# Kernel tuning notes

Measured on AMD Instinct MI355X. Metric: run time of the kernel, lower is better.

## Reference

```python
import jax, jax.numpy as jnp
import numpy as np

N_NODES = 50000
N_EDGES = 600000
N_FEAT = 64
D = 128
N_GRAPHS = 1024
N_LAYERS = 4


def setup_inputs() -> dict:
    key = jax.random.key(0)
    ks = jax.random.split(key, 16)
    x = jax.random.normal(ks[0], (N_NODES, N_FEAT), dtype=jnp.float32)
    edge_index = jax.random.randint(ks[1], (2, N_EDGES), 0, N_NODES, dtype=jnp.int64)
    batch_index = jnp.sort(jax.random.randint(ks[2], (N_NODES,), 0, N_GRAPHS, dtype=jnp.int64))
    def lin(k, fan_in, fan_out):
        s = 1.0 / np.sqrt(fan_in)
        kw, kb = jax.random.split(k)
        w = jax.random.uniform(kw, (fan_in, fan_out), minval=-s, maxval=s, dtype=jnp.float32)
        b = jax.random.uniform(kb, (fan_out,), minval=-s, maxval=s, dtype=jnp.float32)
        return w, b
    w0, b0 = lin(ks[3], N_FEAT, D)
    w1, b1 = lin(ks[4], D, D)
    w2, b2 = lin(ks[5], D, D)
    w3, b3 = lin(ks[6], D, D)
    wp, bp = lin(ks[7], D, D)
    return {"x": x, "edge_index": edge_index, "batch_index": batch_index,
            "w0": w0, "b0": b0, "w1": w1, "b1": b1, "w2": w2, "b2": b2,
            "w3": w3, "b3": b3, "wp": wp, "bp": bp}


def _gin_layer(x, src, dst, w, b):
    # GINConv with eps=0: MLP(x_i + sum_{j in N(i)} x_j); MLP = Linear -> ReLU
    agg = jax.ops.segment_sum(x[src], dst, num_segments=N_NODES)
    return jax.nn.relu((x + agg) @ w + b)


def reference(x, edge_index, batch_index, w0, b0, w1, b1, w2, b2, w3, b3, wp, bp):
    src, dst = edge_index[0], edge_index[1]
    # first layer changes width 64 -> 128; agg happens in input width
    agg0 = jax.ops.segment_sum(x[src], dst, num_segments=N_NODES)
    h = jax.nn.relu((x + agg0) @ w0 + b0)
    for w, b in ((w1, b1), (w2, b2), (w3, b3)):
        h = _gin_layer(h, src, dst, w, b)
    # global mean pool per graph
    sums = jax.ops.segment_sum(h, batch_index, num_segments=N_GRAPHS)
    counts = jax.ops.segment_sum(jnp.ones((N_NODES,), dtype=h.dtype), batch_index, num_segments=N_GRAPHS)
    pooled = sums / jnp.maximum(counts, 1.0)[:, None]
    # post_mp: Linear -> ReLU (dropout identity at inference)
    return jax.nn.relu(pooled @ wp + bp)
```

## Files before the change

kernel.cpp:

```cpp
#include <hip/hip_runtime.h>
#include <hip/hip_fp16.h>


#define N_NODES  50000
#define N_EDGES  600000
#define N_FEAT   64
#define DIM      128
#define N_GRAPHS 1024
#define NB_SCAN  49
#define NBINS    36
#define TPB      256
#define GT128    ((N_NODES + 127) / 128)

typedef _Float16 f16x8 __attribute__((ext_vector_type(8)));
typedef float    f32x4 __attribute__((ext_vector_type(4)));

#define CNTZ  (N_NODES / 4)
#define XWORK (N_NODES * N_FEAT / 4)
#define PREP_TOTAL (CNTZ + XWORK + N_FEAT * DIM + 3 * DIM * DIM)

__global__ __launch_bounds__(TPB) void prep_k(
    const float* __restrict__ x, __half* __restrict__ xh,
    const float* __restrict__ w0, const float* __restrict__ w1,
    const float* __restrict__ w2, const float* __restrict__ w3,
    __half* __restrict__ Wt0, __half* __restrict__ Wt1,
    __half* __restrict__ Wt2, __half* __restrict__ Wt3,
    int* __restrict__ cnt) {
  int i = blockIdx.x * TPB + threadIdx.x;
  if (i < CNTZ) {
    *reinterpret_cast<int4*>(cnt + i * 4) = make_int4(0, 0, 0, 0);
    return;
  }
  i -= CNTZ;
  if (i < XWORK) {
    float4 v = *reinterpret_cast<const float4*>(x + (size_t)i * 4);
    union { __half2 h2[2]; uint2 u; } pk;
    pk.h2[0] = __floats2half2_rn(v.x, v.y);
    pk.h2[1] = __floats2half2_rn(v.z, v.w);
    *reinterpret_cast<uint2*>(xh + (size_t)i * 4) = pk.u;
    return;
  }
  int j = i - XWORK;
  if (j < N_FEAT * DIM) {
    int k = j >> 7, n = j & 127;
    Wt0[n * N_FEAT + k] = __float2half(w0[j]);
    return;
  }
  j -= N_FEAT * DIM;
  if (j >= 3 * DIM * DIM) return;
  int wsel = j / (DIM * DIM);
  int jj = j - wsel * (DIM * DIM);
  int k = jj >> 7, n = jj & 127;
  const float* W = (wsel == 0) ? w1 : (wsel == 1) ? w2 : w3;
  __half* Wt     = (wsel == 0) ? Wt1 : (wsel == 1) ? Wt2 : Wt3;
  Wt[n * DIM + k] = __float2half(W[jj]);
}

__global__ __launch_bounds__(TPB) void hist_k(
    const int* __restrict__ dst, int* __restrict__ cnt) {
  int e = blockIdx.x * TPB + threadIdx.x;
  if (e < N_EDGES) atomicAdd(&cnt[dst[e]], 1);
}

__global__ __launch_bounds__(TPB) void scan_part_k(
    const int* __restrict__ cnt, int* __restrict__ part,
    int* __restrict__ bins) {
  __shared__ int ws[4];
  __shared__ int lbin[NBINS];
  int t = threadIdx.x, b = blockIdx.x;
  if (t < NBINS) lbin[t] = 0;
  __syncthreads();
  int base = b * 1024 + t * 4;
  int s = 0;
  int v[4] = {0, 0, 0, 0};
  if (base + 3 < N_NODES) {
    int4 q = *reinterpret_cast<const int4*>(cnt + base);
    v[0] = q.x; v[1] = q.y; v[2] = q.z; v[3] = q.w;
  } else {
    for (int i = 0; i < 4; ++i) if (base + i < N_NODES) v[i] = cnt[base + i];
  }
#pragma unroll
  for (int i = 0; i < 4; ++i) {
    s += v[i];
    if (base + i < N_NODES) atomicAdd(&lbin[min(v[i], NBINS - 1)], 1);
  }
  for (int off = 32; off; off >>= 1) s += __shfl_down(s, off, 64);
  int lane = t & 63, wv = t >> 6;
  if (lane == 0) ws[wv] = s;
  __syncthreads();
  if (t == 0) part[b] = ws[0] + ws[1] + ws[2] + ws[3];
  if (t < NBINS) bins[b * NBINS + t] = lbin[t];
}

__global__ __launch_bounds__(TPB) void scan_write_k(
    const int* __restrict__ cnt, const int* __restrict__ part,
    const int* __restrict__ bins, int* __restrict__ row_ptr,
    int* __restrict__ fill, int* __restrict__ node_order) {
  __shared__ int wsum[4];
  __shared__ int blk_off_s;
  __shared__ int offj[NBINS];
  __shared__ int lrank[NBINS];
  int t = threadIdx.x, b = blockIdx.x;
  int lane = t & 63, wv = t >> 6;
  int base = b * 1024 + t * 4;

  if (base + 3 < N_NODES)
    *reinterpret_cast<int4*>(fill + base) = make_int4(0, 0, 0, 0);
  else
    for (int i = 0; i < 4; ++i) if (base + i < N_NODES) fill[base + i] = 0;

  if (t < 64) {
    int v = (t < NB_SCAN) ? part[t] : 0;
    int incl = v;
    for (int off = 1; off < 64; off <<= 1) {
      int u = __shfl_up(incl, off, 64);
      if (t >= off) incl += u;
    }
    if (t == b) blk_off_s = incl - v;
  }

  int colbelow = 0, coltot = 0;
  if (t < NBINS) {
    for (int b2 = 0; b2 < NB_SCAN; ++b2) {
      int u = bins[b2 * NBINS + t];
      if (b2 < b) colbelow += u;
      coltot += u;
    }
  }
  if (t < 64) {
    int v = (t < NBINS) ? coltot : 0;
    int incl = v;
    for (int off = 1; off < 64; off <<= 1) {
      int u = __shfl_up(incl, off, 64);
      if (t >= off) incl += u;
    }
    if (t < NBINS) offj[t] = (incl - v) + colbelow;
  }
  if (t < NBINS) lrank[t] = 0;

  int v[4];
#pragma unroll
  for (int i = 0; i < 4; ++i) v[i] = (base + i < N_NODES) ? cnt[base + i] : 0;
  int ls = v[0] + v[1] + v[2] + v[3];
  int incl = ls;
  for (int off = 1; off < 64; off <<= 1) {
    int u = __shfl_up(incl, off, 64);
    if (lane >= off) incl += u;
  }
  if (lane == 63) wsum[wv] = incl;
  __syncthreads();
  int woff = 0;
  for (int w = 0; w < wv; ++w) woff += wsum[w];
  int off0 = blk_off_s + woff + (incl - ls);
  int rp0 = off0, rp1 = off0 + v[0], rp2 = rp1 + v[1], rp3 = rp2 + v[2];
  if (base + 3 < N_NODES)
    *reinterpret_cast<int4*>(row_ptr + base) = make_int4(rp0, rp1, rp2, rp3);
  else {
    int rp[4] = {rp0, rp1, rp2, rp3};
    for (int i = 0; i < 4; ++i) if (base + i < N_NODES) row_ptr[base + i] = rp[i];
  }
  if (b == 0 && t == 0) row_ptr[N_NODES] = N_EDGES;

#pragma unroll
  for (int i = 0; i < 4; ++i) {
    if (base + i < N_NODES) {
      int bin = min(v[i], NBINS - 1);
      int r = atomicAdd(&lrank[bin], 1);
      node_order[offj[bin] + r] = base + i;
    }
  }
}

__global__ __launch_bounds__(TPB) void fill_k(
    const int* __restrict__ src, const int* __restrict__ dst,
    const int* __restrict__ row_ptr, int* __restrict__ fill,
    int* __restrict__ csr_src) {
  int e = blockIdx.x * TPB + threadIdx.x;
  if (e >= N_EDGES) return;
  int d = dst[e];
  int pos = row_ptr[d] + atomicAdd(&fill[d], 1);
  csr_src[pos] = src[e];
}

template<int K, bool EPI>
__global__ __launch_bounds__(TPB) void gemm_k(
    const __half* __restrict__ A, const __half* __restrict__ Wt,
    const float* __restrict__ bias, __half* __restrict__ y) {
  constexpr int KP = K + 8;
  constexpr int OSP = 144;
  constexpr int NKC = K / 32;
  constexpr size_t WSZ = (size_t)128 * KP * sizeof(__half);
  constexpr size_t OSZ = (size_t)128 * OSP * sizeof(__half);
  __shared__ __align__(16) char smem[WSZ > OSZ ? WSZ : OSZ];
  __half (*Ws)[KP]  = reinterpret_cast<__half(*)[KP]>(smem);
  __half (*Os)[OSP] = reinterpret_cast<__half(*)[OSP]>(smem);

  int tid = threadIdx.x;
  int w = tid >> 6, lane = tid & 63;
  int quad = lane >> 4, m = lane & 15;
  int row0 = blockIdx.x * 128;

  for (int i = tid; i < 128 * (K / 8); i += TPB) {
    int r = i / (K / 8), c = (i % (K / 8)) * 8;
    *reinterpret_cast<f16x8*>(&Ws[r][c]) =
        *reinterpret_cast<const f16x8*>(Wt + (size_t)r * K + c);
  }

  f16x8 areg[2][NKC];
#pragma unroll
  for (int s = 0; s < 2; ++s) {
    int row = row0 + w * 32 + s * 16 + m;
    row = min(row, N_NODES - 1);
    const f16x8* Ar = reinterpret_cast<const f16x8*>(A + (size_t)row * K);
#pragma unroll
    for (int kc = 0; kc < NKC; ++kc)
      areg[s][kc] = Ar[kc * 4 + quad];
  }
  __syncthreads();

  f32x4 acc[2][8];
#pragma unroll
  for (int s = 0; s < 2; ++s)
#pragma unroll
    for (int t = 0; t < 8; ++t) acc[s][t] = (f32x4){0.f, 0.f, 0.f, 0.f};

#pragma unroll
  for (int kc = 0; kc < NKC; ++kc) {
#pragma unroll
    for (int t = 0; t < 8; ++t) {
      f16x8 b = *reinterpret_cast<const f16x8*>(&Ws[t * 16 + m][kc * 32 + quad * 8]);
      acc[0][t] = __builtin_amdgcn_mfma_f32_16x16x32_f16(areg[0][kc], b, acc[0][t], 0, 0, 0);
      acc[1][t] = __builtin_amdgcn_mfma_f32_16x16x32_f16(areg[1][kc], b, acc[1][t], 0, 0, 0);
    }
  }

  __syncthreads();

#pragma unroll
  for (int t = 0; t < 8; ++t) {
    float bv = EPI ? bias[t * 16 + m] : 0.f;
#pragma unroll
    for (int s = 0; s < 2; ++s)
#pragma unroll
      for (int r = 0; r < 4; ++r) {
        float v = acc[s][t][r];
        if (EPI) v = fmaxf(v + bv, 0.f);
        Os[w * 32 + s * 16 + quad * 4 + r][t * 16 + m] = __float2half(v);
      }
  }
  __syncthreads();

#pragma unroll
  for (int it = 0; it < 8; ++it) {
    int i = tid + it * TPB;
    int r = i >> 4, c = (i & 15) * 8;
    int row = row0 + r;
    if (row < N_NODES)
      *reinterpret_cast<f16x8*>(y + (size_t)row * 128 + c) =
          *reinterpret_cast<const f16x8*>(&Os[r][c]);
  }
}

template<int F, bool BR>
__global__ __launch_bounds__(TPB) void gather_k(
    const __half* __restrict__ y, const int* __restrict__ row_ptr,
    const int* __restrict__ csr_src, const int* __restrict__ order,
    const float* __restrict__ bias, __half* __restrict__ hout) {
  constexpr int CH = F / 8;
  const f16x8* yv = reinterpret_cast<const f16x8*>(y);
  int gid  = blockIdx.x * TPB + threadIdx.x;
  int rank = gid / CH;
  int l    = gid % CH;
  if (rank >= N_NODES) return;
  int node = order[rank];
  int beg = row_ptr[node], end = row_ptr[node + 1];

  f16x8 self = yv[(size_t)node * CH + l];
  float acc[8];
#pragma unroll
  for (int v = 0; v < 8; ++v) acc[v] = (float)self[v];

  int e = beg;
  for (; e + 3 < end; e += 4) {
    int s0 = csr_src[e+0], s1 = csr_src[e+1], s2 = csr_src[e+2], s3 = csr_src[e+3];
    f16x8 v0 = yv[(size_t)s0 * CH + l];
    f16x8 v1 = yv[(size_t)s1 * CH + l];
    f16x8 v2 = yv[(size_t)s2 * CH + l];
    f16x8 v3 = yv[(size_t)s3 * CH + l];
#pragma unroll
    for (int v = 0; v < 8; ++v)
      acc[v] += ((float)v0[v] + (float)v1[v]) + ((float)v2[v] + (float)v3[v]);
  }
  for (; e < end; ++e) {
    f16x8 v0 = yv[(size_t)csr_src[e] * CH + l];
#pragma unroll
    for (int v = 0; v < 8; ++v) acc[v] += (float)v0[v];
  }

  f16x8 o;
  if (BR) {
    float4 b0 = *reinterpret_cast<const float4*>(bias + l * 8);
    float4 b1 = *reinterpret_cast<const float4*>(bias + l * 8 + 4);
    float bb[8] = {b0.x, b0.y, b0.z, b0.w, b1.x, b1.y, b1.z, b1.w};
#pragma unroll
    for (int v = 0; v < 8; ++v) o[v] = (_Float16)fmaxf(acc[v] + bb[v], 0.f);
  } else {
#pragma unroll
    for (int v = 0; v < 8; ++v) o[v] = (_Float16)acc[v];
  }
  reinterpret_cast<f16x8*>(hout)[(size_t)node * CH + l] = o;
}

__global__ __launch_bounds__(128) void pool_post_k(
    const __half* __restrict__ h, const int* __restrict__ batch,
    const float* __restrict__ W, const float* __restrict__ bias,
    float* __restrict__ out) {
  __shared__ float xs[DIM];
  int g = blockIdx.x;
  int col = threadIdx.x;
  int lo = 0, hi = N_NODES;
  while (lo < hi) { int mid = (lo + hi) >> 1; if (batch[mid] < g) lo = mid + 1; else hi = mid; }
  int beg = lo;
  hi = N_NODES;
  while (lo < hi) { int mid = (lo + hi) >> 1; if (batch[mid] < g + 1) lo = mid + 1; else hi = mid; }
  int end = lo;

  float acc = 0.f;
  for (int n = beg; n < end; ++n) acc += __half2float(h[(size_t)n * DIM + col]);
  float cnt = fmaxf((float)(end - beg), 1.0f);
  xs[col] = acc / cnt;
  __syncthreads();
  float o = bias[col];
  for (int k = 0; k < DIM; ++k)
    o = fmaf(xs[k], W[(size_t)k * DIM + col], o);
  out[(size_t)g * DIM + col] = fmaxf(o, 0.f);
}

extern "C" void kernel_launch(void* const* d_in, const int* in_sizes, int n_in,
                              void* d_out, int out_size, void* d_ws, size_t ws_size,
                              hipStream_t stream) {
  const float* x    = (const float*)d_in[0];
  const int*   ei   = (const int*)d_in[1];
  const int*   batch= (const int*)d_in[2];
  const float* w0 = (const float*)d_in[3];  const float* b0 = (const float*)d_in[4];
  const float* w1 = (const float*)d_in[5];  const float* b1 = (const float*)d_in[6];
  const float* w2 = (const float*)d_in[7];  const float* b2 = (const float*)d_in[8];
  const float* w3 = (const float*)d_in[9];  const float* b3 = (const float*)d_in[10];
  const float* wp = (const float*)d_in[11]; const float* bp = (const float*)d_in[12];
  float* out = (float*)d_out;

  const int* src = ei;
  const int* dst = ei + N_EDGES;

  __half* xh = (__half*)d_ws;
  __half* y  = xh + (size_t)N_NODES * N_FEAT;
  __half* h  = y  + (size_t)N_NODES * DIM;
  __half* Wt0 = h + (size_t)N_NODES * DIM;
  __half* Wt1 = Wt0 + N_FEAT * DIM;
  __half* Wt2 = Wt1 + DIM * DIM;
  __half* Wt3 = Wt2 + DIM * DIM;
  int* cnt     = (int*)(Wt3 + DIM * DIM);
  int* fill    = cnt + N_NODES;
  int* part    = fill + N_NODES;
  int* row_ptr = part + 64;
  int* csr_src = row_ptr + (N_NODES + 1);
  int* node_order = csr_src + N_EDGES;
  int* bins       = node_order + N_NODES;
  __half* s = y;

  prep_k<<<(PREP_TOTAL + TPB - 1) / TPB, TPB, 0, stream>>>(
      x, xh, w0, w1, w2, w3, Wt0, Wt1, Wt2, Wt3, cnt);
  hist_k<<<(N_EDGES + TPB - 1) / TPB, TPB, 0, stream>>>(dst, cnt);
  scan_part_k <<<NB_SCAN, TPB, 0, stream>>>(cnt, part, bins);
  scan_write_k<<<NB_SCAN, TPB, 0, stream>>>(cnt, part, bins, row_ptr, fill,
                                            node_order);
  fill_k<<<(N_EDGES + TPB - 1) / TPB, TPB, 0, stream>>>(src, dst, row_ptr,
                                                        fill, csr_src);

  gather_k<N_FEAT, false><<<(N_NODES * 8 + TPB - 1) / TPB, TPB, 0, stream>>>(
      xh, row_ptr, csr_src, node_order, nullptr, s);
  gemm_k<N_FEAT, true><<<GT128, TPB, 0, stream>>>(s, Wt0, b0, h);

  const __half* Wl[3] = {Wt1, Wt2, Wt3};
  const float*  Bl[3] = {b1, b2, b3};
  for (int l = 0; l < 3; ++l) {
    gemm_k<DIM, false><<<GT128, TPB, 0, stream>>>(h, Wl[l], nullptr, y);
    gather_k<DIM, true><<<(N_NODES * 16 + TPB - 1) / TPB, TPB, 0, stream>>>(
        y, row_ptr, csr_src, node_order, Bl[l], h);
  }

  pool_post_k<<<N_GRAPHS, 128, 0, stream>>>(h, batch, wp, bp, out);
}
```

Baseline: 307.9 us.

## Sort CSR neighbors by source-chunk and drop degree-binned node ordering

The CSR build now keys edges by (dst, src>>13), giving 7 source chunks per node, so each node's neighbor list is grouped by source range. The aim is better L2 locality for the gathers across the four layers. The degree-binned node_order permutation is removed, and gather threads now walk nodes in natural order. In exchange the count, fill and row_ptr arrays become 7x larger, and the scan now covers 350K entries with a 171-block single-pass partial scan. Losing degree sorting may increase load imbalance within waves.

Result: no change. 303.0 us (median of 2 runs) (-1.6%).

```diff
diff --git a/kernel.cpp b/kernel.cpp
--- a/kernel.cpp
+++ b/kernel.cpp
@@ -7,17 +7,20 @@
 #define N_FEAT   64
 #define DIM      128
 #define N_GRAPHS 1024
-#define NB_SCAN  49
-#define NBINS    36
+#define NC       7
+#define CSH      13
+#define TOT2     (N_NODES * NC)
+#define SCH      2048
+#define NBLK     ((TOT2 + SCH - 1) / SCH)
 #define TPB      256
 #define GT128    ((N_NODES + 127) / 128)
 
 typedef _Float16 f16x8 __attribute__((ext_vector_type(8)));
 typedef float    f32x4 __attribute__((ext_vector_type(4)));
 
-#define CNTZ  (N_NODES / 4)
+#define CNTZ2 (TOT2 / 4)
 #define XWORK (N_NODES * N_FEAT / 4)
-#define PREP_TOTAL (CNTZ + XWORK + N_FEAT * DIM + 3 * DIM * DIM)
+#define PREP_TOTAL (CNTZ2 + XWORK + N_FEAT * DIM + 3 * DIM * DIM)
 
 __global__ __launch_bounds__(TPB) void prep_k(
     const float* __restrict__ x, __half* __restrict__ xh,
@@ -25,13 +28,13 @@
     const float* __restrict__ w2, const float* __restrict__ w3,
     __half* __restrict__ Wt0, __half* __restrict__ Wt1,
     __half* __restrict__ Wt2, __half* __restrict__ Wt3,
-    int* __restrict__ cnt) {
+    int* __restrict__ cnt2) {
   int i = blockIdx.x * TPB + threadIdx.x;
-  if (i < CNTZ) {
-    *reinterpret_cast<int4*>(cnt + i * 4) = make_int4(0, 0, 0, 0);
+  if (i < CNTZ2) {
+    *reinterpret_cast<int4*>(cnt2 + i * 4) = make_int4(0, 0, 0, 0);
     return;
   }
-  i -= CNTZ;
+  i -= CNTZ2;
   if (i < XWORK) {
     float4 v = *reinterpret_cast<const float4*>(x + (size_t)i * 4);
     union { __half2 h2[2]; uint2 u; } pk;
@@ -57,91 +60,66 @@
 }
 
 __global__ __launch_bounds__(TPB) void hist_k(
-    const int* __restrict__ dst, int* __restrict__ cnt) {
+    const int* __restrict__ src, const int* __restrict__ dst,
+    int* __restrict__ cnt2) {
   int e = blockIdx.x * TPB + threadIdx.x;
-  if (e < N_EDGES) atomicAdd(&cnt[dst[e]], 1);
+  if (e >= N_EDGES) return;
+  int key = dst[e] * NC + (src[e] >> CSH);
+  atomicAdd(&cnt2[key], 1);
 }
 
 __global__ __launch_bounds__(TPB) void scan_part_k(
-    const int* __restrict__ cnt, int* __restrict__ part,
-    int* __restrict__ bins) {
+    const int* __restrict__ cnt2, int* __restrict__ part) {
   __shared__ int ws[4];
-  __shared__ int lbin[NBINS];
   int t = threadIdx.x, b = blockIdx.x;
-  if (t < NBINS) lbin[t] = 0;
-  __syncthreads();
-  int base = b * 1024 + t * 4;
+  int base = b * SCH + t * 8;
   int s = 0;
-  int v[4] = {0, 0, 0, 0};
-  if (base + 3 < N_NODES) {
-    int4 q = *reinterpret_cast<const int4*>(cnt + base);
-    v[0] = q.x; v[1] = q.y; v[2] = q.z; v[3] = q.w;
-  } else {
-    for (int i = 0; i < 4; ++i) if (base + i < N_NODES) v[i] = cnt[base + i];
-  }
-#pragma unroll
-  for (int i = 0; i < 4; ++i) {
-    s += v[i];
-    if (base + i < N_NODES) atomicAdd(&lbin[min(v[i], NBINS - 1)], 1);
+  if (base < TOT2) {
+    int4 a = *reinterpret_cast<const int4*>(cnt2 + base);
+    int4 c = *reinterpret_cast<const int4*>(cnt2 + base + 4);
+    s = a.x + a.y + a.z + a.w + c.x + c.y + c.z + c.w;
   }
   for (int off = 32; off; off >>= 1) s += __shfl_down(s, off, 64);
   int lane = t & 63, wv = t >> 6;
   if (lane == 0) ws[wv] = s;
   __syncthreads();
   if (t == 0) part[b] = ws[0] + ws[1] + ws[2] + ws[3];
-  if (t < NBINS) bins[b * NBINS + t] = lbin[t];
 }
 
 __global__ __launch_bounds__(TPB) void scan_write_k(
-    const int* __restrict__ cnt, const int* __restrict__ part,
-    const int* __restrict__ bins, int* __restrict__ row_ptr,
-    int* __restrict__ fill, int* __restrict__ node_order) {
+    const int* __restrict__ cnt2, const int* __restrict__ part,
+    int* __restrict__ row_ptr2, int* __restrict__ fill2) {
+  __shared__ int pscan[TPB];
   __shared__ int wsum[4];
-  __shared__ int blk_off_s;
-  __shared__ int offj[NBINS];
-  __shared__ int lrank[NBINS];
   int t = threadIdx.x, b = blockIdx.x;
   int lane = t & 63, wv = t >> 6;
-  int base = b * 1024 + t * 4;
-
-  if (base + 3 < N_NODES)
-    *reinterpret_cast<int4*>(fill + base) = make_int4(0, 0, 0, 0);
-  else
-    for (int i = 0; i < 4; ++i) if (base + i < N_NODES) fill[base + i] = 0;
-
-  if (t < 64) {
-    int v = (t < NB_SCAN) ? part[t] : 0;
-    int incl = v;
-    for (int off = 1; off < 64; off <<= 1) {
-      int u = __shfl_up(incl, off, 64);
-      if (t >= off) incl += u;
-    }
-    if (t == b) blk_off_s = incl - v;
-  }
-
-  int colbelow = 0, coltot = 0;
-  if (t < NBINS) {
-    for (int b2 = 0; b2 < NB_SCAN; ++b2) {
-      int u = bins[b2 * NBINS + t];
-      if (b2 < b) colbelow += u;
-      coltot += u;
-    }
-  }
-  if (t < 64) {
-    int v = (t < NBINS) ? coltot : 0;
-    int incl = v;
-    for (int off = 1; off < 64; off <<= 1) {
-      int u = __shfl_up(incl, off, 64);
-      if (t >= off) incl += u;
-    }
-    if (t < NBINS) offj[t] = (incl - v) + colbelow;
-  }
-  if (t < NBINS) lrank[t] = 0;
-
-  int v[4];
-#pragma unroll
-  for (int i = 0; i < 4; ++i) v[i] = (base + i < N_NODES) ? cnt[base + i] : 0;
-  int ls = v[0] + v[1] + v[2] + v[3];
+  int base = b * SCH + t * 8;
+
+  if (base < TOT2) {
+    *reinterpret_cast<int4*>(fill2 + base) = make_int4(0, 0, 0, 0);
+    *reinterpret_cast<int4*>(fill2 + base + 4) = make_int4(0, 0, 0, 0);
+  }
+
+  pscan[t] = (t < NBLK) ? part[t] : 0;
+  __syncthreads();
+  for (int off = 1; off < TPB; off <<= 1) {
+    int v = (t >= off) ? pscan[t - off] : 0;
+    __syncthreads();
+    pscan[t] += v;
+    __syncthreads();
+  }
+  int blk_off = (b > 0) ? pscan[b - 1] : 0;
+
+  int v[8] = {0,0,0,0,0,0,0,0};
+  if (base < TOT2) {
+    int4 a = *reinterpret_cast<const int4*>(cnt2 + base);
+    int4 c = *reinterpret_cast<const int4*>(cnt2 + base + 4);
+    v[0]=a.x; v[1]=a.y; v[2]=a.z; v[3]=a.w;
+    v[4]=c.x; v[5]=c.y; v[6]=c.z; v[7]=c.w;
+  }
+  int ls = 0;
+#pragma unroll
+  for (int i = 0; i < 8; ++i) ls += v[i];
   int incl = ls;
   for (int off = 1; off < 64; off <<= 1) {
     int u = __shfl_up(incl, off, 64);
@@ -151,35 +129,27 @@
   __syncthreads();
   int woff = 0;
   for (int w = 0; w < wv; ++w) woff += wsum[w];
-  int off0 = blk_off_s + woff + (incl - ls);
-  int rp0 = off0, rp1 = off0 + v[0], rp2 = rp1 + v[1], rp3 = rp2 + v[2];
-  if (base + 3 < N_NODES)
-    *reinterpret_cast<int4*>(row_ptr + base) = make_int4(rp0, rp1, rp2, rp3);
-  else {
-    int rp[4] = {rp0, rp1, rp2, rp3};
-    for (int i = 0; i < 4; ++i) if (base + i < N_NODES) row_ptr[base + i] = rp[i];
-  }
-  if (b == 0 && t == 0) row_ptr[N_NODES] = N_EDGES;
-
-#pragma unroll
-  for (int i = 0; i < 4; ++i) {
-    if (base + i < N_NODES) {
-      int bin = min(v[i], NBINS - 1);
-      int r = atomicAdd(&lrank[bin], 1);
-      node_order[offj[bin] + r] = base + i;
-    }
-  }
+  int run = blk_off + woff + (incl - ls);
+  if (base < TOT2) {
+    int rp[8];
+#pragma unroll
+    for (int i = 0; i < 8; ++i) { rp[i] = run; run += v[i]; }
+    *reinterpret_cast<int4*>(row_ptr2 + base) = make_int4(rp[0], rp[1], rp[2], rp[3]);
+    *reinterpret_cast<int4*>(row_ptr2 + base + 4) = make_int4(rp[4], rp[5], rp[6], rp[7]);
+  }
+  if (b == 0 && t == 0) row_ptr2[TOT2] = N_EDGES;
 }
 
 __global__ __launch_bounds__(TPB) void fill_k(
     const int* __restrict__ src, const int* __restrict__ dst,
-    const int* __restrict__ row_ptr, int* __restrict__ fill,
+    const int* __restrict__ row_ptr2, int* __restrict__ fill2,
     int* __restrict__ csr_src) {
   int e = blockIdx.x * TPB + threadIdx.x;
   if (e >= N_EDGES) return;
-  int d = dst[e];
-  int pos = row_ptr[d] + atomicAdd(&fill[d], 1);
-  csr_src[pos] = src[e];
+  int s = src[e];
+  int key = dst[e] * NC + (s >> CSH);
+  int pos = row_ptr2[key] + atomicAdd(&fill2[key], 1);
+  csr_src[pos] = s;
 }
 
 template<int K, bool EPI>
@@ -263,17 +233,17 @@
 
 template<int F, bool BR>
 __global__ __launch_bounds__(TPB) void gather_k(
-    const __half* __restrict__ y, const int* __restrict__ row_ptr,
-    const int* __restrict__ csr_src, const int* __restrict__ order,
-    const float* __restrict__ bias, __half* __restrict__ hout) {
+    const __half* __restrict__ y, const int* __restrict__ row_ptr2,
+    const int* __restrict__ csr_src, const float* __restrict__ bias,
+    __half* __restrict__ hout) {
   constexpr int CH = F / 8;
   const f16x8* yv = reinterpret_cast<const f16x8*>(y);
   int gid  = blockIdx.x * TPB + threadIdx.x;
-  int rank = gid / CH;
+  int node = gid / CH;
   int l    = gid % CH;
-  if (rank >= N_NODES) return;
-  int node = order[rank];
-  int beg = row_ptr[node], end = row_ptr[node + 1];
+  if (node >= N_NODES) return;
+  int beg = row_ptr2[node * NC];
+  int end = row_ptr2[node * NC + NC];
 
   f16x8 self = yv[(size_t)node * CH + l];
   float acc[8];
@@ -359,26 +329,23 @@
   __half* Wt1 = Wt0 + N_FEAT * DIM;
   __half* Wt2 = Wt1 + DIM * DIM;
   __half* Wt3 = Wt2 + DIM * DIM;
-  int* cnt     = (int*)(Wt3 + DIM * DIM);
-  int* fill    = cnt + N_NODES;
-  int* part    = fill + N_NODES;
-  int* row_ptr = part + 64;
-  int* csr_src = row_ptr + (N_NODES + 1);
-  int* node_order = csr_src + N_EDGES;
-  int* bins       = node_order + N_NODES;
+  int* cnt2     = (int*)(Wt3 + DIM * DIM);
+  int* fill2    = cnt2 + TOT2;
+  int* part     = fill2 + TOT2;
+  int* row_ptr2 = part + 256;
+  int* csr_src  = row_ptr2 + (TOT2 + 1);
   __half* s = y;
 
   prep_k<<<(PREP_TOTAL + TPB - 1) / TPB, TPB, 0, stream>>>(
-      x, xh, w0, w1, w2, w3, Wt0, Wt1, Wt2, Wt3, cnt);
-  hist_k<<<(N_EDGES + TPB - 1) / TPB, TPB, 0, stream>>>(dst, cnt);
-  scan_part_k <<<NB_SCAN, TPB, 0, stream>>>(cnt, part, bins);
-  scan_write_k<<<NB_SCAN, TPB, 0, stream>>>(cnt, part, bins, row_ptr, fill,
-                                            node_order);
-  fill_k<<<(N_EDGES + TPB - 1) / TPB, TPB, 0, stream>>>(src, dst, row_ptr,
-                                                        fill, csr_src);
+      x, xh, w0, w1, w2, w3, Wt0, Wt1, Wt2, Wt3, cnt2);
+  hist_k<<<(N_EDGES + TPB - 1) / TPB, TPB, 0, stream>>>(src, dst, cnt2);
+  scan_part_k <<<NBLK, TPB, 0, stream>>>(cnt2, part);
+  scan_write_k<<<NBLK, TPB, 0, stream>>>(cnt2, part, row_ptr2, fill2);
+  fill_k<<<(N_EDGES + TPB - 1) / TPB, TPB, 0, stream>>>(src, dst, row_ptr2,
+                                                        fill2, csr_src);
 
   gather_k<N_FEAT, false><<<(N_NODES * 8 + TPB - 1) / TPB, TPB, 0, stream>>>(
-      xh, row_ptr, csr_src, node_order, nullptr, s);
+      xh, row_ptr2, csr_src, nullptr, s);
   gemm_k<N_FEAT, true><<<GT128, TPB, 0, stream>>>(s, Wt0, b0, h);
 
   const __half* Wl[3] = {Wt1, Wt2, Wt3};
@@ -386,7 +353,7 @@
   for (int l = 0; l < 3; ++l) {
     gemm_k<DIM, false><<<GT128, TPB, 0, stream>>>(h, Wl[l], nullptr, y);
     gather_k<DIM, true><<<(N_NODES * 16 + TPB - 1) / TPB, TPB, 0, stream>>>(
-        y, row_ptr, csr_src, node_order, Bl[l], h);
+        y, row_ptr2, csr_src, Bl[l], h);
   }
 
   pool_post_k<<<N_GRAPHS, 128, 0, stream>>>(h, batch, wp, bp, out);
```
